# Performance work log

Hardware: AMD Instinct MI355X
Metric: run time of the kernel (lower is better)

## Reference

```python
import jax, jax.numpy as jnp
import numpy as np

NUM_ENTITIES = 100000
NUM_RELATIONS = 500
DIM = 512
CHANNELS = 32
KERNEL = 3
BATCH = 2048


def setup_inputs() -> dict:
    key = jax.random.key(0)
    ks = jax.random.split(key, 9)
    # xavier_uniform bounds
    b_ent = float(np.sqrt(6.0 / (NUM_ENTITIES + DIM)))
    b_rel = float(np.sqrt(6.0 / (NUM_RELATIONS + DIM)))
    ent = jax.random.uniform(ks[0], (NUM_ENTITIES, DIM), jnp.float32, -b_ent, b_ent)
    rel = jax.random.uniform(ks[1], (NUM_RELATIONS, DIM), jnp.float32, -b_rel, b_rel)
    # Conv1d(1, CHANNELS, KERNEL) default init: U(-s, s), s = 1/sqrt(in_ch*k)
    s_conv = float(1.0 / np.sqrt(1 * KERNEL))
    conv_w = jax.random.uniform(ks[2], (CHANNELS, 1, KERNEL), jnp.float32, -s_conv, s_conv)
    conv_b = jax.random.uniform(ks[3], (CHANNELS,), jnp.float32, -s_conv, s_conv)
    # Linear(CHANNELS*DIM, DIM)
    s_proj = float(1.0 / np.sqrt(CHANNELS * DIM))
    proj_w = jax.random.uniform(ks[4], (DIM, CHANNELS * DIM), jnp.float32, -s_proj, s_proj)
    proj_b = jax.random.uniform(ks[5], (DIM,), jnp.float32, -s_proj, s_proj)
    h = jax.random.randint(ks[6], (BATCH,), 0, NUM_ENTITIES, jnp.int32)
    r = jax.random.randint(ks[7], (BATCH,), 0, NUM_RELATIONS, jnp.int32)
    t = jax.random.randint(ks[8], (BATCH,), 0, NUM_ENTITIES, jnp.int32)
    return {"h": h, "r": r, "t": t, "ent": ent, "rel": rel,
            "conv_w": conv_w, "conv_b": conv_b, "proj_w": proj_w, "proj_b": proj_b}


def reference(h, r, t, ent, rel, conv_w, conv_b, proj_w, proj_b):
    dim = ent.shape[1]
    h_e = ent[h]                                   # [B, D]
    r_e = rel[r]                                   # [B, D]
    x = jnp.concatenate([h_e, r_e], axis=-1)[:, None, :]   # [B, 1, 2D]
    x = jax.lax.conv_general_dilated(
        x, conv_w, window_strides=(1,), padding='SAME',
        dimension_numbers=('NCH', 'OIH', 'NCH'))   # [B, C, 2D]
    x = jax.nn.relu(x + conv_b[None, :, None])
    x = x[..., :dim]                               # [B, C, D]
    x = x.reshape(x.shape[0], -1)                  # [B, C*D]
    x = x @ proj_w.T + proj_b                      # [B, D]
    scores = x @ ent.T                             # [B, N] full-entity scores
    return scores[jnp.arange(t.shape[0]), t]       # [B]
```

## Files before the change

### kernel.cpp

```cpp
#include <hip/hip_runtime.h>

#define DIM    512
#define CH     32
#define KDIM   16384
#define BATCH  2048
#define NOUT   512
#define PWN    (NOUT * KDIM)

#define BM 128
#define BN 128
#define BK 32
#define KSPLIT 4
#define KC (KDIM / KSPLIT)

typedef short bf16x8 __attribute__((ext_vector_type(8)));
typedef float f32x4  __attribute__((ext_vector_type(4)));

__device__ __forceinline__ float b2f(unsigned short u) {
    union { unsigned int i; float f; } v; v.i = ((unsigned int)u) << 16; return v.f;
}
__device__ __forceinline__ unsigned short f2b(float f) {
    union { float f; unsigned int i; } v; v.f = f;
    unsigned int r = v.i + 0x7fffu + ((v.i >> 16) & 1u);
    return (unsigned short)(r >> 16);
}
__device__ __forceinline__ float ldv(const void* p, size_t i, int isf) {
    return isf ? ((const float*)p)[i] : b2f(((const unsigned short*)p)[i]);
}

__global__ void sniff_kernel(const unsigned short* __restrict__ ent_raw,
                             int* __restrict__ flag) {
    int lane = threadIdx.x;
    unsigned short u = ent_raw[2 * lane];
    int eb = (u >> 8) & 0x7F;
    int hit = (eb >= 0x36 && eb < 0x3C) ? 1 : 0;
    #pragma unroll
    for (int o = 32; o; o >>= 1) hit += __shfl_xor(hit, o, 64);
    if (lane == 0) *flag = (hit < 32) ? 1 : 0;
}

__global__ __launch_bounds__(256) void convert_kernel(
    const void* __restrict__ projw, unsigned short* __restrict__ pw16,
    const int* __restrict__ flagp) {
    const int isf = *flagp;
    size_t i0 = ((size_t)blockIdx.x * 256 + threadIdx.x) * 4;
    if (i0 >= PWN) return;
    if (isf) {
        f32x4 v = *(const f32x4*)((const float*)projw + i0);
        unsigned int p0 = (unsigned int)f2b(v[0]) | ((unsigned int)f2b(v[1]) << 16);
        unsigned int p1 = (unsigned int)f2b(v[2]) | ((unsigned int)f2b(v[3]) << 16);
        *(unsigned int*)(pw16 + i0) = p0;
        *(unsigned int*)(pw16 + i0 + 2) = p1;
    } else {
        *(unsigned long long*)(pw16 + i0) =
            *(const unsigned long long*)((const unsigned short*)projw + i0);
    }
}

__global__ __launch_bounds__(256) void feat_kernel(
    const int* __restrict__ h, const int* __restrict__ r,
    const void* __restrict__ ent, const void* __restrict__ rel,
    const void* __restrict__ conv_w, const void* __restrict__ conv_b,
    unsigned short* __restrict__ feat, const int* __restrict__ flagp)
{
    __shared__ float xs[DIM + 2];
    __shared__ float wS[CH][4];
    const int b   = blockIdx.x;
    const int tid = threadIdx.x;
    const int isf = *flagp;

    const size_t hb = (size_t)h[b] * DIM;
    for (int j = tid; j < DIM; j += 256) xs[1 + j] = ldv(ent, hb + j, isf);
    if (tid == 0) xs[0] = 0.0f;
    if (tid == 1) xs[DIM + 1] = ldv(rel, (size_t)r[b] * DIM, isf);
    if (tid >= 64 && tid < 96) {
        int c = tid - 64;
        wS[c][0] = ldv(conv_w, c * 3 + 0, isf);
        wS[c][1] = ldv(conv_w, c * 3 + 1, isf);
        wS[c][2] = ldv(conv_w, c * 3 + 2, isf);
        wS[c][3] = ldv(conv_b, c, isf);
    }
    __syncthreads();

    unsigned short* fb = feat + (size_t)b * KDIM;
    const int i0 = tid * 2;
    float x0 = xs[i0], x1 = xs[i0 + 1], x2 = xs[i0 + 2], x3 = xs[i0 + 3];
    #pragma unroll 8
    for (int c = 0; c < CH; ++c) {
        float w0 = wS[c][0], w1 = wS[c][1], w2 = wS[c][2], cb = wS[c][3];
        float v0 = fmaxf(fmaf(w0, x0, fmaf(w1, x1, fmaf(w2, x2, cb))), 0.0f);
        float v1 = fmaxf(fmaf(w0, x1, fmaf(w1, x2, fmaf(w2, x3, cb))), 0.0f);
        unsigned int pack = (unsigned int)f2b(v0) | ((unsigned int)f2b(v1) << 16);
        *(unsigned int*)&fb[c * DIM + i0] = pack;
    }
}

__global__ __launch_bounds__(256, 2) void gemm_kernel(
    const unsigned short* __restrict__ feat,
    const unsigned short* __restrict__ pw16,
    float* __restrict__ Xp)
{
    __shared__ __align__(16) unsigned short As[BM * BK];
    __shared__ __align__(16) unsigned short Bs[BN * BK];

    const int tid  = threadIdx.x;
    const int lane = tid & 63;
    const int wave = tid >> 6;
    const int wm = wave & 1;
    const int wn = wave >> 1;
    const int bx = blockIdx.x, by = blockIdx.y, bz = blockIdx.z;

    const unsigned short* Ab = feat + (size_t)(bx * BM) * KDIM + bz * KC;
    const unsigned short* Bb = pw16 + (size_t)(by * BN) * KDIM + bz * KC;

    const int row_ld = tid >> 2;
    const int koff   = (tid & 3) * 8;

    const f32x4 zero = {0.f, 0.f, 0.f, 0.f};
    f32x4 acc[4][4];
    #pragma unroll
    for (int i = 0; i < 4; ++i)
        #pragma unroll
        for (int j = 0; j < 4; ++j) acc[i][j] = zero;

    const int fRow = lane & 15;
    const int fK   = (lane >> 4) * 8;

    for (int kk = 0; kk < KC; kk += BK) {
        bf16x8 a0 = *(const bf16x8*)(Ab + (size_t)row_ld * KDIM + kk + koff);
        bf16x8 a1 = *(const bf16x8*)(Ab + (size_t)(row_ld + 64) * KDIM + kk + koff);
        bf16x8 b0 = *(const bf16x8*)(Bb + (size_t)row_ld * KDIM + kk + koff);
        bf16x8 b1 = *(const bf16x8*)(Bb + (size_t)(row_ld + 64) * KDIM + kk + koff);
        __syncthreads();
        *(bf16x8*)&As[row_ld * BK + koff]        = a0;
        *(bf16x8*)&As[(row_ld + 64) * BK + koff] = a1;
        *(bf16x8*)&Bs[row_ld * BK + koff]        = b0;
        *(bf16x8*)&Bs[(row_ld + 64) * BK + koff] = b1;
        __syncthreads();

        bf16x8 af[4], bfr[4];
        #pragma unroll
        for (int mi = 0; mi < 4; ++mi)
            af[mi] = *(const bf16x8*)&As[(wm * 64 + mi * 16 + fRow) * BK + fK];
        #pragma unroll
        for (int ni = 0; ni < 4; ++ni)
            bfr[ni] = *(const bf16x8*)&Bs[(wn * 64 + ni * 16 + fRow) * BK + fK];
        #pragma unroll
        for (int mi = 0; mi < 4; ++mi)
            #pragma unroll
            for (int ni = 0; ni < 4; ++ni)
                acc[mi][ni] = __builtin_amdgcn_mfma_f32_16x16x32_bf16(
                    af[mi], bfr[ni], acc[mi][ni], 0, 0, 0);
    }

    float* Xs = Xp + (size_t)bz * BATCH * NOUT;
    const int rbase = bx * BM + wm * 64 + (lane >> 4) * 4;
    const int cbase = by * BN + wn * 64 + (lane & 15);
    #pragma unroll
    for (int mi = 0; mi < 4; ++mi)
        #pragma unroll
        for (int ni = 0; ni < 4; ++ni)
            #pragma unroll
            for (int rr = 0; rr < 4; ++rr) {
                int row = rbase + mi * 16 + rr;
                int col = cbase + ni * 16;
                Xs[(size_t)row * NOUT + col] = acc[mi][ni][rr];
            }
}

__global__ __launch_bounds__(256) void score_kernel(
    const int* __restrict__ t, const void* __restrict__ ent,
    const float* __restrict__ Xp, const void* __restrict__ projb,
    void* __restrict__ out, const int* __restrict__ flagp)
{
    const int lane = threadIdx.x & 63;
    const int wave = threadIdx.x >> 6;
    const int b = blockIdx.x * 4 + wave;
    const int isf = *flagp;
    const size_t tb = (size_t)t[b] * DIM;
    float s = 0.f;
    #pragma unroll
    for (int j = 0; j < 8; ++j) {
        int d = lane + 64 * j;
        float xp = ldv(projb, d, isf);
        #pragma unroll
        for (int z = 0; z < KSPLIT; ++z)
            xp += Xp[(size_t)z * BATCH * NOUT + (size_t)b * NOUT + d];
        s += xp * ldv(ent, tb + d, isf);
    }
    #pragma unroll
    for (int o = 32; o; o >>= 1) s += __shfl_xor(s, o, 64);
    if (lane == 0) {
        if (isf) ((float*)out)[b] = s;
        else     ((unsigned short*)out)[b] = f2b(s);
    }
}

extern "C" void kernel_launch(void* const* d_in, const int* in_sizes, int n_in,
                              void* d_out, int out_size, void* d_ws, size_t ws_size,
                              hipStream_t stream)
{
    const int* h = (const int*)d_in[0];
    const int* r = (const int*)d_in[1];
    const int* t = (const int*)d_in[2];
    const void* ent    = d_in[3];
    const void* rel    = d_in[4];
    const void* conv_w = d_in[5];
    const void* conv_b = d_in[6];
    const void* projw  = d_in[7];
    const void* projb  = d_in[8];

    unsigned short* feat = (unsigned short*)d_ws;
    unsigned short* pw16 = (unsigned short*)((char*)d_ws + (size_t)BATCH * KDIM * 2);
    float* Xp = (float*)((char*)pw16 + (size_t)PWN * 2);
    int* flag = (int*)((char*)Xp + (size_t)KSPLIT * BATCH * NOUT * 4);

    sniff_kernel<<<1, 64, 0, stream>>>((const unsigned short*)ent, flag);
    convert_kernel<<<(PWN / 4 + 255) / 256, 256, 0, stream>>>(projw, pw16, flag);
    feat_kernel<<<BATCH, 256, 0, stream>>>(h, r, ent, rel, conv_w, conv_b, feat, flag);
    gemm_kernel<<<dim3(BATCH / BM, NOUT / BN, KSPLIT), 256, 0, stream>>>(feat, pw16, Xp);
    score_kernel<<<BATCH / 4, 256, 0, stream>>>(t, ent, Xp, projb, d_out, flag);
}
```

Baseline: 361.5 us.

## Load GEMM tiles directly to LDS, double split-K, inline dtype sniffing

The GEMM's global-to-register-to-LDS staging is replaced with direct global_load_lds transfers, and the split-K factor goes from 4 to 8 so more workgroups run in parallel. The separate sniff kernel is removed; each kernel now detects the dtype itself with a wavefront ballot, saving one launch and the flag round-trip. Costs: the score kernel reads twice as many partial sums and the Xp workspace doubles. The direct-to-LDS path loses the register prefetch overlap, and a trailing barrier was added so the next load cannot overwrite tiles still being read.

```diff
diff --git a/kernel.cpp b/kernel.cpp
--- a/kernel.cpp
+++ b/kernel.cpp
@@ -10,7 +10,7 @@
 #define BM 128
 #define BN 128
 #define BK 32
-#define KSPLIT 4
+#define KSPLIT 8
 #define KC (KDIM / KSPLIT)
 
 typedef short bf16x8 __attribute__((ext_vector_type(8)));
@@ -27,22 +27,25 @@
 __device__ __forceinline__ float ldv(const void* p, size_t i, int isf) {
     return isf ? ((const float*)p)[i] : b2f(((const unsigned short*)p)[i]);
 }
-
-__global__ void sniff_kernel(const unsigned short* __restrict__ ent_raw,
-                             int* __restrict__ flag) {
-    int lane = threadIdx.x;
+__device__ __forceinline__ int sniff_isf32(const unsigned short* ent_raw) {
+    int lane = threadIdx.x & 63;
     unsigned short u = ent_raw[2 * lane];
     int eb = (u >> 8) & 0x7F;
-    int hit = (eb >= 0x36 && eb < 0x3C) ? 1 : 0;
-    #pragma unroll
-    for (int o = 32; o; o >>= 1) hit += __shfl_xor(hit, o, 64);
-    if (lane == 0) *flag = (hit < 32) ? 1 : 0;
+    unsigned long long m = __ballot(eb >= 0x36 && eb < 0x3C);
+    return (__popcll(m) < 32) ? 1 : 0;
+}
+
+__device__ __forceinline__ void gload_lds16(const unsigned short* g, unsigned short* l) {
+    __builtin_amdgcn_global_load_lds(
+        (const __attribute__((address_space(1))) void*)g,
+        (__attribute__((address_space(3))) void*)l,
+        16, 0, 0);
 }
 
 __global__ __launch_bounds__(256) void convert_kernel(
     const void* __restrict__ projw, unsigned short* __restrict__ pw16,
-    const int* __restrict__ flagp) {
-    const int isf = *flagp;
+    const unsigned short* __restrict__ ent_raw) {
+    const int isf = sniff_isf32(ent_raw);
     size_t i0 = ((size_t)blockIdx.x * 256 + threadIdx.x) * 4;
     if (i0 >= PWN) return;
     if (isf) {
@@ -61,13 +64,13 @@
     const int* __restrict__ h, const int* __restrict__ r,
     const void* __restrict__ ent, const void* __restrict__ rel,
     const void* __restrict__ conv_w, const void* __restrict__ conv_b,
-    unsigned short* __restrict__ feat, const int* __restrict__ flagp)
+    unsigned short* __restrict__ feat)
 {
     __shared__ float xs[DIM + 2];
     __shared__ float wS[CH][4];
     const int b   = blockIdx.x;
     const int tid = threadIdx.x;
-    const int isf = *flagp;
+    const int isf = sniff_isf32((const unsigned short*)ent);
 
     const size_t hb = (size_t)h[b] * DIM;
     for (int j = tid; j < DIM; j += 256) xs[1 + j] = ldv(ent, hb + j, isf);
@@ -127,15 +130,10 @@
     const int fK   = (lane >> 4) * 8;
 
     for (int kk = 0; kk < KC; kk += BK) {
-        bf16x8 a0 = *(const bf16x8*)(Ab + (size_t)row_ld * KDIM + kk + koff);
-        bf16x8 a1 = *(const bf16x8*)(Ab + (size_t)(row_ld + 64) * KDIM + kk + koff);
-        bf16x8 b0 = *(const bf16x8*)(Bb + (size_t)row_ld * KDIM + kk + koff);
-        bf16x8 b1 = *(const bf16x8*)(Bb + (size_t)(row_ld + 64) * KDIM + kk + koff);
-        __syncthreads();
-        *(bf16x8*)&As[row_ld * BK + koff]        = a0;
-        *(bf16x8*)&As[(row_ld + 64) * BK + koff] = a1;
-        *(bf16x8*)&Bs[row_ld * BK + koff]        = b0;
-        *(bf16x8*)&Bs[(row_ld + 64) * BK + koff] = b1;
+        gload_lds16(Ab + (size_t)row_ld * KDIM + kk + koff,        As + row_ld * BK + koff);
+        gload_lds16(Ab + (size_t)(row_ld + 64) * KDIM + kk + koff, As + (row_ld + 64) * BK + koff);
+        gload_lds16(Bb + (size_t)row_ld * KDIM + kk + koff,        Bs + row_ld * BK + koff);
+        gload_lds16(Bb + (size_t)(row_ld + 64) * KDIM + kk + koff, Bs + (row_ld + 64) * BK + koff);
         __syncthreads();
 
         bf16x8 af[4], bfr[4];
@@ -151,6 +149,7 @@
             for (int ni = 0; ni < 4; ++ni)
                 acc[mi][ni] = __builtin_amdgcn_mfma_f32_16x16x32_bf16(
                     af[mi], bfr[ni], acc[mi][ni], 0, 0, 0);
+        __syncthreads();
     }
 
     float* Xs = Xp + (size_t)bz * BATCH * NOUT;
@@ -171,12 +170,12 @@
 __global__ __launch_bounds__(256) void score_kernel(
     const int* __restrict__ t, const void* __restrict__ ent,
     const float* __restrict__ Xp, const void* __restrict__ projb,
-    void* __restrict__ out, const int* __restrict__ flagp)
+    void* __restrict__ out)
 {
     const int lane = threadIdx.x & 63;
     const int wave = threadIdx.x >> 6;
     const int b = blockIdx.x * 4 + wave;
-    const int isf = *flagp;
+    const int isf = sniff_isf32((const unsigned short*)ent);
     const size_t tb = (size_t)t[b] * DIM;
     float s = 0.f;
     #pragma unroll
@@ -213,11 +212,9 @@
     unsigned short* feat = (unsigned short*)d_ws;
     unsigned short* pw16 = (unsigned short*)((char*)d_ws + (size_t)BATCH * KDIM * 2);
     float* Xp = (float*)((char*)pw16 + (size_t)PWN * 2);
-    int* flag = (int*)((char*)Xp + (size_t)KSPLIT * BATCH * NOUT * 4);
-
-    sniff_kernel<<<1, 64, 0, stream>>>((const unsigned short*)ent, flag);
-    convert_kernel<<<(PWN / 4 + 255) / 256, 256, 0, stream>>>(projw, pw16, flag);
-    feat_kernel<<<BATCH, 256, 0, stream>>>(h, r, ent, rel, conv_w, conv_b, feat, flag);
+
+    convert_kernel<<<(PWN / 4 + 255) / 256, 256, 0, stream>>>(projw, pw16, (const unsigned short*)ent);
+    feat_kernel<<<BATCH, 256, 0, stream>>>(h, r, ent, rel, conv_w, conv_b, feat);
     gemm_kernel<<<dim3(BATCH / BM, NOUT / BN, KSPLIT), 256, 0, stream>>>(feat, pw16, Xp);
-    score_kernel<<<BATCH / 4, 256, 0, stream>>>(t, ent, Xp, projb, d_out, flag);
-}
+    score_kernel<<<BATCH / 4, 256, 0, stream>>>(t, ent, Xp, projb, d_out);
+}
```

Measured after the change: 336.4 us. -6.9%, faster.
